# Kernel optimization log

Measured on AMD Instinct MI355X. Metric: run time of the kernel, lower is better.

The kernel has to match this reference:

```python
import jax, jax.numpy as jnp
import numpy as np

B, PRE, NEXT, DIN, DOUT = 256, 64, 32, 128, 64


def _squash(x):
    # x: [..., D]; scale = |x|^2/(1+|x|^2) * x/|x|
    s2 = jnp.sum(x * x, axis=-1, keepdims=True)
    return (s2 / (1.0 + s2)) * x / jnp.sqrt(s2 + 1e-8)


def setup_inputs() -> dict:
    key = jax.random.key(0)
    kx, kw = jax.random.split(key)
    x = jax.random.normal(kx, (B, PRE, DIN), dtype=jnp.float32)
    W = jax.random.normal(kw, (PRE, NEXT, DIN, DOUT), dtype=jnp.float32)
    return {"x": x, "W": W, "iter_time": 3}


def reference(x, W, iter_time):
    Bn = x.shape[0]
    k, K, _, D = W.shape
    # pose predictions: [B, k, K, D]
    p = jnp.einsum('bkd,kKdD->bkKD', x, W)
    b = jnp.zeros((Bn, k, K), dtype=x.dtype)
    q = jnp.zeros((Bn, K, D), dtype=x.dtype)
    for _ in range(iter_time):
        c = jax.nn.softmax(b, axis=-1)                 # [B,k,K]
        q = _squash(jnp.einsum('bkKD,bkK->bKD', p, c))  # [B,K,D]
        b = b + jnp.einsum('bkKD,bKD->bkK', p, q)
    return q.reshape(Bn, -1)
```

## Files before the change

### kernel.cpp

```cpp
#include <hip/hip_runtime.h>
#include <math.h>

#define BATCH 256
#define PRE   64
#define NEXT  32
#define DIN   128
#define DOUT  64

typedef __attribute__((ext_vector_type(8))) short bf16x8;
typedef __attribute__((ext_vector_type(4))) float f32x4;

__device__ __forceinline__ unsigned short f2bf(float f) {
    unsigned u = __float_as_uint(f);
    unsigned r = (u + 0x7fffu + ((u >> 16) & 1u)) >> 16;
    return (unsigned short)r;
}
__device__ __forceinline__ float bf2f(unsigned short h) {
    return __uint_as_float(((unsigned)h) << 16);
}

#define WFRAG_S 10

__global__ __launch_bounds__(256, 2) void gemm_kernel(const float* __restrict__ x,
                                                      const float* __restrict__ W,
                                                      float* __restrict__ p,
                                                      int b0)
{
    __shared__ float xs[128 * 40];
    __shared__ unsigned wpk[256 * WFRAG_S];
    const int K    = blockIdx.x;
    const int kk   = blockIdx.y;
    const int bt   = blockIdx.z;
    const int t    = threadIdx.x;
    const int wave = t >> 6;
    const int lane = t & 63;
    const int ln   = lane & 15;
    const int quad = lane >> 4;
    const int row0 = bt * 128 + wave * 32;

    f32x4 acc[2][4];
#pragma unroll
    for (int mt = 0; mt < 2; ++mt)
#pragma unroll
        for (int nt = 0; nt < 4; ++nt) acc[mt][nt] = (f32x4){0.f, 0.f, 0.f, 0.f};

    const float* Wk = W + (size_t)(kk * NEXT + K) * DIN * DOUT;

    for (int dc = 0; dc < 4; ++dc) {
        __syncthreads();
#pragma unroll
        for (int i = 0; i < 4; ++i) {
            const int f   = t + 256 * i;
            const int row = f >> 3;
            const int d4  = f & 7;
            float4 v = *(const float4*)(x + ((size_t)(b0 + bt * 128 + row) * PRE + kk) * DIN + dc * 32 + d4 * 4);
            *(float4*)&xs[row * 40 + d4 * 4] = v;
        }
#pragma unroll
        for (int it = 0; it < 8; ++it) {
            const int e  = it * 256 + t;
            const int dl = e >> 6;
            const int D  = e & 63;
            float v = Wk[(size_t)(dc * 32 + dl) * DOUT + D];
            unsigned short h = f2bf(v);
            unsigned short l = f2bf(v - bf2f(h));
            const int fr = ((D >> 4) * 64 + (dl >> 3) * 16 + (D & 15));
            wpk[fr * WFRAG_S + (dl & 7)] = (unsigned)h | ((unsigned)l << 16);
        }
        __syncthreads();

        bf16x8 ah[2], al[2];
#pragma unroll
        for (int mt = 0; mt < 2; ++mt) {
            const float* xa = &xs[(wave * 32 + mt * 16 + ln) * 40 + quad * 8];
            float4 v0 = *(const float4*)xa;
            float4 v1 = *(const float4*)(xa + 4);
            float xv[8] = {v0.x, v0.y, v0.z, v0.w, v1.x, v1.y, v1.z, v1.w};
#pragma unroll
            for (int j = 0; j < 8; ++j) {
                unsigned short h = f2bf(xv[j]);
                ah[mt][j] = (short)h;
                al[mt][j] = (short)f2bf(xv[j] - bf2f(h));
            }
        }
        bf16x8 bh[4], bl[4];
#pragma unroll
        for (int nt = 0; nt < 4; ++nt) {
            const unsigned* wp = &wpk[(nt * 64 + quad * 16 + ln) * WFRAG_S];
            unsigned pk[8];
#pragma unroll
            for (int i2 = 0; i2 < 4; ++i2) *(uint2*)&pk[i2 * 2] = *(const uint2*)&wp[i2 * 2];
            union { bf16x8 v; unsigned u[4]; } BH, BL;
#pragma unroll
            for (int i2 = 0; i2 < 4; ++i2) {
                BH.u[i2] = (pk[2 * i2] & 0xffffu) | (pk[2 * i2 + 1] << 16);
                BL.u[i2] = (pk[2 * i2] >> 16) | (pk[2 * i2 + 1] & 0xffff0000u);
            }
            bh[nt] = BH.v; bl[nt] = BL.v;
        }
#pragma unroll
        for (int mt = 0; mt < 2; ++mt)
#pragma unroll
            for (int nt = 0; nt < 4; ++nt) {
                acc[mt][nt] = __builtin_amdgcn_mfma_f32_16x16x32_bf16(ah[mt], bh[nt], acc[mt][nt], 0, 0, 0);
                acc[mt][nt] = __builtin_amdgcn_mfma_f32_16x16x32_bf16(al[mt], bh[nt], acc[mt][nt], 0, 0, 0);
                acc[mt][nt] = __builtin_amdgcn_mfma_f32_16x16x32_bf16(ah[mt], bl[nt], acc[mt][nt], 0, 0, 0);
            }
    }

#pragma unroll
    for (int mt = 0; mt < 2; ++mt)
#pragma unroll
        for (int nt = 0; nt < 4; ++nt) {
            const int D = nt * 16 + ln;
#pragma unroll
            for (int r = 0; r < 4; ++r) {
                const int row = row0 + mt * 16 + quad * 4 + r;
                p[((size_t)(row * PRE + kk) * NEXT + K) * DOUT + D] = acc[mt][nt][r];
            }
        }
}

#define QSTR 68
#define QBUF (32 * QSTR)

__global__ __launch_bounds__(1024, 1) void route_kernel(const float* __restrict__ p,
                                                        float* __restrict__ out,
                                                        int b0)
{
    __shared__ float qpart[8 * QBUF];
    __shared__ float qsum[QBUF];
    const int b    = blockIdx.x;
    const int t    = threadIdx.x;
    const int w    = t >> 6;
    const int lane = t & 63;
    const int g    = lane >> 4;
    const int m    = lane & 15;
    const float4* pb = (const float4*)(p + (size_t)b * (PRE * NEXT * DOUT));

    for (int idx = t; idx < QBUF; idx += 1024) qsum[idx] = 0.f;
    __syncthreads();

    for (int pass = 0; pass < 3; ++pass) {
        float4 qa[8];
#pragma unroll
        for (int j = 0; j < 8; ++j) qa[j] = (float4){0.f, 0.f, 0.f, 0.f};

        float4 pv[2][8];
        {
            const size_t sb = (size_t)w * 512;
#pragma unroll
            for (int j = 0; j < 8; ++j) pv[0][j] = pb[sb + j * 64 + lane];
        }
#pragma unroll
        for (int i = 0; i < 4; ++i) {
            const int buf = i & 1;
            if (i < 3) {
                const size_t sb = (size_t)((i + 1) * 16 + w) * 512;
#pragma unroll
                for (int j = 0; j < 8; ++j) pv[buf ^ 1][j] = pb[sb + j * 64 + lane];
            }
            float c[8];
            if (pass == 0) {
#pragma unroll
                for (int j = 0; j < 8; ++j) c[j] = 1.0f / 32.0f;
            } else {
#pragma unroll
                for (int j = 0; j < 8; ++j) {
                    float4 qv = *(const float4*)&qsum[(j * 4 + g) * QSTR + m * 4];
                    float d = pv[buf][j].x * qv.x + pv[buf][j].y * qv.y
                            + pv[buf][j].z * qv.z + pv[buf][j].w * qv.w;
                    d += __shfl_xor(d, 1);
                    d += __shfl_xor(d, 2);
                    d += __shfl_xor(d, 4);
                    d += __shfl_xor(d, 8);
                    c[j] = d;
                }
                float mx = c[0];
#pragma unroll
                for (int j = 1; j < 8; ++j) mx = fmaxf(mx, c[j]);
                mx = fmaxf(mx, __shfl_xor(mx, 16));
                mx = fmaxf(mx, __shfl_xor(mx, 32));
                float s = 0.f;
#pragma unroll
                for (int j = 0; j < 8; ++j) { c[j] = __expf(c[j] - mx); s += c[j]; }
                s += __shfl_xor(s, 16);
                s += __shfl_xor(s, 32);
                float inv = 1.0f / s;
#pragma unroll
                for (int j = 0; j < 8; ++j) c[j] *= inv;
            }
#pragma unroll
            for (int j = 0; j < 8; ++j) {
                qa[j].x += c[j] * pv[buf][j].x;
                qa[j].y += c[j] * pv[buf][j].y;
                qa[j].z += c[j] * pv[buf][j].z;
                qa[j].w += c[j] * pv[buf][j].w;
            }
        }
        if (w < 8) {
#pragma unroll
            for (int j = 0; j < 8; ++j)
                *(float4*)&qpart[w * QBUF + (j * 4 + g) * QSTR + m * 4] = qa[j];
        }
        __syncthreads();
        if (w >= 8) {
#pragma unroll
            for (int j = 0; j < 8; ++j) {
                float* qd = &qpart[(w - 8) * QBUF + (j * 4 + g) * QSTR + m * 4];
                float4 old = *(const float4*)qd;
                old.x += qa[j].x; old.y += qa[j].y; old.z += qa[j].z; old.w += qa[j].w;
                *(float4*)qd = old;
            }
        }
        __syncthreads();

        {
            const int Kq = t >> 5, pr = t & 31;
            float vx = 0.f, vy = 0.f;
#pragma unroll
            for (int ww = 0; ww < 8; ++ww) {
                const float* s2p = &qpart[ww * QBUF + Kq * QSTR + pr * 2];
                vx += s2p[0]; vy += s2p[1];
            }
            float s2 = vx * vx + vy * vy;
            s2 += __shfl_xor(s2, 1);
            s2 += __shfl_xor(s2, 2);
            s2 += __shfl_xor(s2, 4);
            s2 += __shfl_xor(s2, 8);
            s2 += __shfl_xor(s2, 16);
            float fsc = s2 / ((1.f + s2) * sqrtf(s2 + 1e-8f));
            vx *= fsc; vy *= fsc;
            if (pass < 2) {
                float* qd = &qsum[Kq * QSTR + pr * 2];
                qd[0] += vx; qd[1] += vy;
            } else {
                float* od = out + (size_t)(b0 + b) * 2048 + Kq * 64 + pr * 2;
                od[0] = vx; od[1] = vy;
            }
        }
        if (pass < 2) __syncthreads();
    }
}

extern "C" void kernel_launch(void* const* d_in, const int* in_sizes, int n_in,
                              void* d_out, int out_size, void* d_ws, size_t ws_size,
                              hipStream_t stream) {
    const float* x = (const float*)d_in[0];
    const float* W = (const float*)d_in[1];
    float* out = (float*)d_out;
    float* p   = (float*)d_ws;

    const int chunk = (ws_size >= (size_t)134217728) ? 256 : 128;

    for (int b0 = 0; b0 < BATCH; b0 += chunk) {
        gemm_kernel<<<dim3(NEXT, PRE, chunk / 128), 256, 0, stream>>>(x, W, p, b0);
        route_kernel<<<chunk, 1024, 0, stream>>>(p, out, b0);
    }
}
```

Baseline: 251.1 us.

## Process two output capsules per GEMM block to reuse x split fragments

Each GEMM block now computes two adjacent K capsules, so the staged x tile and its bf16 hi/lo split are reused across both W slabs, and the grid is halved. W fragments are stored in separate hi and lo LDS arrays already packed in MFMA order, which removes the per-fragment unpack shuffles. The cost is twice the accumulators per thread (more register pressure at 2 blocks/SM), fewer blocks overall, and a larger LDS footprint.

```diff
diff --git a/kernel.cpp b/kernel.cpp
--- a/kernel.cpp
+++ b/kernel.cpp
@@ -18,8 +18,6 @@
 __device__ __forceinline__ float bf2f(unsigned short h) {
     return __uint_as_float(((unsigned)h) << 16);
 }
-
-#define WFRAG_S 10
 
 __global__ __launch_bounds__(256, 2) void gemm_kernel(const float* __restrict__ x,
                                                       const float* __restrict__ W,
@@ -27,8 +25,9 @@
                                                       int b0)
 {
     __shared__ float xs[128 * 40];
-    __shared__ unsigned wpk[256 * WFRAG_S];
-    const int K    = blockIdx.x;
+    __shared__ unsigned bhw[2][256 * 6];
+    __shared__ unsigned blw[2][256 * 6];
+    const int Kp2  = blockIdx.x;
     const int kk   = blockIdx.y;
     const int bt   = blockIdx.z;
     const int t    = threadIdx.x;
@@ -36,15 +35,16 @@
     const int lane = t & 63;
     const int ln   = lane & 15;
     const int quad = lane >> 4;
-    const int row0 = bt * 128 + wave * 32;
-
-    f32x4 acc[2][4];
+
+    f32x4 acc[2][2][4];
 #pragma unroll
     for (int mt = 0; mt < 2; ++mt)
 #pragma unroll
-        for (int nt = 0; nt < 4; ++nt) acc[mt][nt] = (f32x4){0.f, 0.f, 0.f, 0.f};
-
-    const float* Wk = W + (size_t)(kk * NEXT + K) * DIN * DOUT;
+        for (int s = 0; s < 2; ++s)
+#pragma unroll
+            for (int nt = 0; nt < 4; ++nt) acc[mt][s][nt] = (f32x4){0.f, 0.f, 0.f, 0.f};
+
+    const float* Wk0 = W + (size_t)(kk * NEXT + Kp2 * 2) * DIN * DOUT;
 
     for (int dc = 0; dc < 4; ++dc) {
         __syncthreads();
@@ -58,14 +58,21 @@
         }
 #pragma unroll
         for (int it = 0; it < 8; ++it) {
-            const int e  = it * 256 + t;
-            const int dl = e >> 6;
-            const int D  = e & 63;
-            float v = Wk[(size_t)(dc * 32 + dl) * DOUT + D];
-            unsigned short h = f2bf(v);
-            unsigned short l = f2bf(v - bf2f(h));
-            const int fr = ((D >> 4) * 64 + (dl >> 3) * 16 + (D & 15));
-            wpk[fr * WFRAG_S + (dl & 7)] = (unsigned)h | ((unsigned)l << 16);
+            const int slab = it >> 2;
+            const int e    = (it & 3) * 256 + t;
+            const int D    = e & 63;
+            const int dlp  = e >> 6;
+            const float* wb = Wk0 + (size_t)slab * (DIN * DOUT)
+                            + (size_t)(dc * 32 + dlp * 2) * DOUT + D;
+            float v0 = wb[0];
+            float v1 = wb[DOUT];
+            unsigned short h0 = f2bf(v0), h1 = f2bf(v1);
+            unsigned short l0 = f2bf(v0 - bf2f(h0));
+            unsigned short l1 = f2bf(v1 - bf2f(h1));
+            const int fr = (D >> 4) * 64 + (dlp >> 2) * 16 + (D & 15);
+            const int wi = fr * 6 + (dlp & 3);
+            bhw[slab][wi] = (unsigned)h0 | ((unsigned)h1 << 16);
+            blw[slab][wi] = (unsigned)l0 | ((unsigned)l1 << 16);
         }
         __syncthreads();
 
@@ -83,42 +90,40 @@
                 al[mt][j] = (short)f2bf(xv[j] - bf2f(h));
             }
         }
-        bf16x8 bh[4], bl[4];
 #pragma unroll
         for (int nt = 0; nt < 4; ++nt) {
-            const unsigned* wp = &wpk[(nt * 64 + quad * 16 + ln) * WFRAG_S];
-            unsigned pk[8];
-#pragma unroll
-            for (int i2 = 0; i2 < 4; ++i2) *(uint2*)&pk[i2 * 2] = *(const uint2*)&wp[i2 * 2];
-            union { bf16x8 v; unsigned u[4]; } BH, BL;
-#pragma unroll
-            for (int i2 = 0; i2 < 4; ++i2) {
-                BH.u[i2] = (pk[2 * i2] & 0xffffu) | (pk[2 * i2 + 1] << 16);
-                BL.u[i2] = (pk[2 * i2] >> 16) | (pk[2 * i2 + 1] & 0xffff0000u);
-            }
-            bh[nt] = BH.v; bl[nt] = BL.v;
-        }
-#pragma unroll
-        for (int mt = 0; mt < 2; ++mt)
+            const int fr = nt * 64 + quad * 16 + ln;
+#pragma unroll
+            for (int s = 0; s < 2; ++s) {
+                const uint2* hp = (const uint2*)&bhw[s][fr * 6];
+                const uint2* lp = (const uint2*)&blw[s][fr * 6];
+                union { bf16x8 v; uint2 u[2]; } BH, BL;
+                BH.u[0] = hp[0]; BH.u[1] = hp[1];
+                BL.u[0] = lp[0]; BL.u[1] = lp[1];
+#pragma unroll
+                for (int mt = 0; mt < 2; ++mt) {
+                    acc[mt][s][nt] = __builtin_amdgcn_mfma_f32_16x16x32_bf16(ah[mt], BH.v, acc[mt][s][nt], 0, 0, 0);
+                    acc[mt][s][nt] = __builtin_amdgcn_mfma_f32_16x16x32_bf16(al[mt], BH.v, acc[mt][s][nt], 0, 0, 0);
+                    acc[mt][s][nt] = __builtin_amdgcn_mfma_f32_16x16x32_bf16(ah[mt], BL.v, acc[mt][s][nt], 0, 0, 0);
+                }
+            }
+        }
+    }
+
+#pragma unroll
+    for (int mt = 0; mt < 2; ++mt)
+#pragma unroll
+        for (int s = 0; s < 2; ++s)
 #pragma unroll
             for (int nt = 0; nt < 4; ++nt) {
-                acc[mt][nt] = __builtin_amdgcn_mfma_f32_16x16x32_bf16(ah[mt], bh[nt], acc[mt][nt], 0, 0, 0);
-                acc[mt][nt] = __builtin_amdgcn_mfma_f32_16x16x32_bf16(al[mt], bh[nt], acc[mt][nt], 0, 0, 0);
-                acc[mt][nt] = __builtin_amdgcn_mfma_f32_16x16x32_bf16(ah[mt], bl[nt], acc[mt][nt], 0, 0, 0);
-            }
-    }
-
-#pragma unroll
-    for (int mt = 0; mt < 2; ++mt)
-#pragma unroll
-        for (int nt = 0; nt < 4; ++nt) {
-            const int D = nt * 16 + ln;
-#pragma unroll
-            for (int r = 0; r < 4; ++r) {
-                const int row = row0 + mt * 16 + quad * 4 + r;
-                p[((size_t)(row * PRE + kk) * NEXT + K) * DOUT + D] = acc[mt][nt][r];
-            }
-        }
+                const int D = nt * 16 + ln;
+                const int K = Kp2 * 2 + s;
+#pragma unroll
+                for (int r = 0; r < 4; ++r) {
+                    const int row = bt * 128 + wave * 32 + mt * 16 + quad * 4 + r;
+                    p[((size_t)(row * PRE + kk) * NEXT + K) * DOUT + D] = acc[mt][s][nt][r];
+                }
+            }
 }
 
 #define QSTR 68
@@ -254,7 +259,7 @@
     const int chunk = (ws_size >= (size_t)134217728) ? 256 : 128;
 
     for (int b0 = 0; b0 < BATCH; b0 += chunk) {
-        gemm_kernel<<<dim3(NEXT, PRE, chunk / 128), 256, 0, stream>>>(x, W, p, b0);
+        gemm_kernel<<<dim3(NEXT / 2, PRE, chunk / 128), 256, 0, stream>>>(x, W, p, b0);
         route_kernel<<<chunk, 1024, 0, stream>>>(p, out, b0);
     }
 }
```

Result: slower. 289.1 us (+15.1%).

## Fuse first routing pass into GEMM epilogue via atomic accumulation

Applied to the files above, without the earlier changes.

The GEMM epilogue now also atomically adds each pose prediction into the output buffer, which is cleared first with a memset. This buffer then holds the per-capsule sum over input capsules. The routing kernel reads that sum, scales it by the uniform coefficient and squashes it to get the first q, so it runs two passes over p instead of three. This removes one full read of the large p tensor. In exchange the GEMM issues one float atomic per output element, with 64-way contention per address, plus an extra memset.

```diff
diff --git a/kernel.cpp b/kernel.cpp
--- a/kernel.cpp
+++ b/kernel.cpp
@@ -24,6 +24,7 @@
 __global__ __launch_bounds__(256, 2) void gemm_kernel(const float* __restrict__ x,
                                                       const float* __restrict__ W,
                                                       float* __restrict__ p,
+                                                      float* __restrict__ s0,
                                                       int b0)
 {
     __shared__ float xs[128 * 40];
@@ -116,7 +117,9 @@
 #pragma unroll
             for (int r = 0; r < 4; ++r) {
                 const int row = row0 + mt * 16 + quad * 4 + r;
-                p[((size_t)(row * PRE + kk) * NEXT + K) * DOUT + D] = acc[mt][nt][r];
+                const float v = acc[mt][nt][r];
+                p[((size_t)(row * PRE + kk) * NEXT + K) * DOUT + D] = v;
+                atomicAdd(&s0[(size_t)(b0 + row) * 2048 + K * 64 + D], v);
             }
         }
 }
@@ -138,10 +141,24 @@
     const int m    = lane & 15;
     const float4* pb = (const float4*)(p + (size_t)b * (PRE * NEXT * DOUT));
 
-    for (int idx = t; idx < QBUF; idx += 1024) qsum[idx] = 0.f;
+    {
+        const int Kq = t >> 5, pr = t & 31;
+        const float* s0p = out + (size_t)(b0 + b) * 2048 + Kq * 64 + pr * 2;
+        float vx = s0p[0] * (1.0f / 32.0f);
+        float vy = s0p[1] * (1.0f / 32.0f);
+        float s2 = vx * vx + vy * vy;
+        s2 += __shfl_xor(s2, 1);
+        s2 += __shfl_xor(s2, 2);
+        s2 += __shfl_xor(s2, 4);
+        s2 += __shfl_xor(s2, 8);
+        s2 += __shfl_xor(s2, 16);
+        float fsc = s2 / ((1.f + s2) * sqrtf(s2 + 1e-8f));
+        float* qd = &qsum[Kq * QSTR + pr * 2];
+        qd[0] = vx * fsc; qd[1] = vy * fsc;
+    }
     __syncthreads();
 
-    for (int pass = 0; pass < 3; ++pass) {
+    for (int pass = 0; pass < 2; ++pass) {
         float4 qa[8];
 #pragma unroll
         for (int j = 0; j < 8; ++j) qa[j] = (float4){0.f, 0.f, 0.f, 0.f};
@@ -161,35 +178,30 @@
                 for (int j = 0; j < 8; ++j) pv[buf ^ 1][j] = pb[sb + j * 64 + lane];
             }
             float c[8];
-            if (pass == 0) {
-#pragma unroll
-                for (int j = 0; j < 8; ++j) c[j] = 1.0f / 32.0f;
-            } else {
-#pragma unroll
-                for (int j = 0; j < 8; ++j) {
-                    float4 qv = *(const float4*)&qsum[(j * 4 + g) * QSTR + m * 4];
-                    float d = pv[buf][j].x * qv.x + pv[buf][j].y * qv.y
-                            + pv[buf][j].z * qv.z + pv[buf][j].w * qv.w;
-                    d += __shfl_xor(d, 1);
-                    d += __shfl_xor(d, 2);
-                    d += __shfl_xor(d, 4);
-                    d += __shfl_xor(d, 8);
-                    c[j] = d;
-                }
-                float mx = c[0];
-#pragma unroll
-                for (int j = 1; j < 8; ++j) mx = fmaxf(mx, c[j]);
-                mx = fmaxf(mx, __shfl_xor(mx, 16));
-                mx = fmaxf(mx, __shfl_xor(mx, 32));
-                float s = 0.f;
-#pragma unroll
-                for (int j = 0; j < 8; ++j) { c[j] = __expf(c[j] - mx); s += c[j]; }
-                s += __shfl_xor(s, 16);
-                s += __shfl_xor(s, 32);
-                float inv = 1.0f / s;
-#pragma unroll
-                for (int j = 0; j < 8; ++j) c[j] *= inv;
-            }
+#pragma unroll
+            for (int j = 0; j < 8; ++j) {
+                float4 qv = *(const float4*)&qsum[(j * 4 + g) * QSTR + m * 4];
+                float d = pv[buf][j].x * qv.x + pv[buf][j].y * qv.y
+                        + pv[buf][j].z * qv.z + pv[buf][j].w * qv.w;
+                d += __shfl_xor(d, 1);
+                d += __shfl_xor(d, 2);
+                d += __shfl_xor(d, 4);
+                d += __shfl_xor(d, 8);
+                c[j] = d;
+            }
+            float mx = c[0];
+#pragma unroll
+            for (int j = 1; j < 8; ++j) mx = fmaxf(mx, c[j]);
+            mx = fmaxf(mx, __shfl_xor(mx, 16));
+            mx = fmaxf(mx, __shfl_xor(mx, 32));
+            float s = 0.f;
+#pragma unroll
+            for (int j = 0; j < 8; ++j) { c[j] = __expf(c[j] - mx); s += c[j]; }
+            s += __shfl_xor(s, 16);
+            s += __shfl_xor(s, 32);
+            float inv = 1.0f / s;
+#pragma unroll
+            for (int j = 0; j < 8; ++j) c[j] *= inv;
 #pragma unroll
             for (int j = 0; j < 8; ++j) {
                 qa[j].x += c[j] * pv[buf][j].x;
@@ -231,7 +243,7 @@
             s2 += __shfl_xor(s2, 16);
             float fsc = s2 / ((1.f + s2) * sqrtf(s2 + 1e-8f));
             vx *= fsc; vy *= fsc;
-            if (pass < 2) {
+            if (pass == 0) {
                 float* qd = &qsum[Kq * QSTR + pr * 2];
                 qd[0] += vx; qd[1] += vy;
             } else {
@@ -239,7 +251,7 @@
                 od[0] = vx; od[1] = vy;
             }
         }
-        if (pass < 2) __syncthreads();
+        if (pass == 0) __syncthreads();
     }
 }
 
@@ -254,7 +266,9 @@
     const int chunk = (ws_size >= (size_t)134217728) ? 256 : 128;
 
     for (int b0 = 0; b0 < BATCH; b0 += chunk) {
-        gemm_kernel<<<dim3(NEXT, PRE, chunk / 128), 256, 0, stream>>>(x, W, p, b0);
+        hipMemsetAsync((char*)out + (size_t)b0 * 2048 * 4, 0,
+                       (size_t)chunk * 2048 * 4, stream);
+        gemm_kernel<<<dim3(NEXT, PRE, chunk / 128), 256, 0, stream>>>(x, W, p, out, b0);
         route_kernel<<<chunk, 1024, 0, stream>>>(p, out, b0);
     }
 }
```

Measured after the change: 333.5 us. +32.8%, slower.
